# Performance work log

Hardware: AMD Instinct MI355X
Metric: run time of the kernel (lower is better)

Reference implementation:

```python
import jax, jax.numpy as jnp
import numpy as np

N_UNITS = 1024
H = 16
D_K = N_UNITS // H
B = 4
T = 2048


def setup_inputs() -> dict:
    key = jax.random.key(0)
    ks = jax.random.split(key, 9)
    scale = 1.0 / np.sqrt(N_UNITS)
    return {
        "x": jax.random.normal(ks[0], (B * T, N_UNITS), dtype=jnp.float32),
        "Wq": jax.random.normal(ks[1], (N_UNITS, N_UNITS), dtype=jnp.float32) * scale,
        "bq": jax.random.normal(ks[2], (N_UNITS,), dtype=jnp.float32) * 0.01,
        "Wk": jax.random.normal(ks[3], (N_UNITS, N_UNITS), dtype=jnp.float32) * scale,
        "bk": jax.random.normal(ks[4], (N_UNITS,), dtype=jnp.float32) * 0.01,
        "Wv": jax.random.normal(ks[5], (N_UNITS, N_UNITS), dtype=jnp.float32) * scale,
        "bv": jax.random.normal(ks[6], (N_UNITS,), dtype=jnp.float32) * 0.01,
        "Wo": jax.random.normal(ks[7], (N_UNITS, N_UNITS), dtype=jnp.float32) * scale,
        "bo": jax.random.normal(ks[8], (N_UNITS,), dtype=jnp.float32) * 0.01,
        "batch_size": B,
    }


def reference(x, Wq, bq, Wk, bk, Wv, bv, Wo, bo, batch_size):
    # x: (batch*seq, n_units). Project then split into heads.
    q = (x @ Wq.T + bq).reshape(batch_size, -1, H, D_K)  # (b, t, h, d)
    k = (x @ Wk.T + bk).reshape(batch_size, -1, H, D_K)
    v = (x @ Wv.T + bv).reshape(batch_size, -1, H, D_K)
    scores = jnp.einsum("bqhd,bkhd->bhqk", q, k) / np.sqrt(D_K)
    att = jax.nn.softmax(scores, axis=-1)  # dropout=0.0 -> identity
    ctx = jnp.einsum("bhqk,bkhd->bqhd", att, v)
    ctx = ctx.reshape(-1, H * D_K)  # (batch*seq, n_units)
    return ctx @ Wo.T + bo
```

## Files before the change

### kernel.cpp

```cpp
#include <hip/hip_runtime.h>

typedef __bf16 bf16_t;
typedef __attribute__((ext_vector_type(8))) __bf16 bf16x8;
typedef __attribute__((ext_vector_type(4))) __bf16 bf16x4;
typedef __attribute__((ext_vector_type(4))) float f32x4;

#define M_TOT 8192
#define NU    1024
#define TSEQ  2048
#define NHEAD 16
#define DHEAD 64
#define BPAD  72
#define QSCALE 0.18033688011f

__device__ __forceinline__ void gload_lds16(const void* g, void* lds) {
    __builtin_amdgcn_global_load_lds(
        (const __attribute__((address_space(1))) void*)g,
        (__attribute__((address_space(3))) void*)lds,
        16, 0, 0);
}

__device__ __forceinline__ unsigned pk2(float a, float b) {
    const bf16_t x = (bf16_t)a, y = (bf16_t)b;
    return (unsigned)__builtin_bit_cast(unsigned short, x)
         | ((unsigned)__builtin_bit_cast(unsigned short, y) << 16);
}

__device__ __forceinline__ int fidx(int r, int k) {
    return ((((r >> 4) & 3) * 2 + (k >> 5)) << 9)
         + (((((k >> 3) & 3) << 4) + (r & 15)) << 3) + (k & 7);
}
__device__ __forceinline__ size_t fragK(int bh, int t, int d) {
    return (size_t)bh * (TSEQ * DHEAD) + (size_t)(t >> 6) * 4096 + fidx(t & 63, d);
}
__device__ __forceinline__ size_t fragV(int bh, int t, int d) {
    return (size_t)bh * (TSEQ * DHEAD) + (size_t)(t >> 6) * 4096 + fidx(d, t & 63);
}

__global__ __launch_bounds__(256)
void cvt_x(const float* __restrict__ x, bf16_t* __restrict__ xb)
{
    const int i = (blockIdx.x * 256 + threadIdx.x) * 8;
    const float4 a = *(const float4*)(x + i);
    const float4 b = *(const float4*)(x + i + 4);
    bf16x8 v;
    v[0] = (bf16_t)a.x; v[1] = (bf16_t)a.y; v[2] = (bf16_t)a.z; v[3] = (bf16_t)a.w;
    v[4] = (bf16_t)b.x; v[5] = (bf16_t)b.y; v[6] = (bf16_t)b.z; v[7] = (bf16_t)b.w;
    *(bf16x8*)(xb + i) = v;
}

__global__ __launch_bounds__(256)
void cvt_frag2(const float* __restrict__ x,
               const float* __restrict__ Wq, const float* __restrict__ Wk,
               const float* __restrict__ Wv, const float* __restrict__ Wo,
               bf16_t* __restrict__ Xf, bf16_t* __restrict__ Wf4)
{
    const int bid = blockIdx.x;
    const float* src;
    bf16_t* dst;
    int trow, tcol;
    if (bid < 2048) {
        src = x;
        dst = Xf + (size_t)bid * 4096;
        trow = bid >> 4; tcol = bid & 15;
    } else {
        const int t    = bid - 2048;
        const int wsel = t >> 8;
        const int tt   = t & 255;
        src = (wsel == 0) ? Wq : (wsel == 1 ? Wk : (wsel == 2 ? Wv : Wo));
        dst = Wf4 + (size_t)wsel * NU * NU + (size_t)tt * 4096;
        trow = tt >> 4; tcol = tt & 15;
    }
    const size_t row0 = (size_t)trow * 64;
    const int    col0 = tcol * 64;

    const int tid = threadIdx.x;
#pragma unroll
    for (int h = 0; h < 2; ++h) {
        const int chunk = h * 256 + tid;
        const int r  = chunk >> 3;
        const int k8 = chunk & 7;
        const float* s = src + (row0 + r) * NU + col0 + k8 * 8;
        const float4 a = *(const float4*)(s);
        const float4 b = *(const float4*)(s + 4);
        bf16x8 v;
        v[0] = (bf16_t)a.x; v[1] = (bf16_t)a.y; v[2] = (bf16_t)a.z; v[3] = (bf16_t)a.w;
        v[4] = (bf16_t)b.x; v[5] = (bf16_t)b.y; v[6] = (bf16_t)b.z; v[7] = (bf16_t)b.w;
        const int idx = ((((r >> 4) & 3) * 2 + (k8 >> 2)) << 9)
                      + (((k8 & 3) * 16 + (r & 15)) << 3);
        *(bf16x8*)(dst + idx) = v;
    }
}

__global__ __launch_bounds__(256)
void gemm_qkv_f(const bf16_t* __restrict__ xf,
                const bf16_t* __restrict__ Wqf, const bf16_t* __restrict__ Wkf, const bf16_t* __restrict__ Wvf,
                const float* __restrict__ B0, const float* __restrict__ B1, const float* __restrict__ B2,
                bf16_t* __restrict__ O0, bf16_t* __restrict__ O1, bf16_t* __restrict__ O2)
{
    const int z = blockIdx.z;
    const bf16_t* Wf  = (z == 0) ? Wqf : (z == 1 ? Wkf : Wvf);
    const float* bias = (z == 0) ? B0 : (z == 1 ? B1 : B2);
    bf16_t* out       = (z == 0) ? O0 : (z == 1 ? O1 : O2);
    const float scale = (z == 0) ? QSCALE : 1.0f;

    __shared__ __attribute__((aligned(16))) bf16_t S[2][16384];

    const int tid = threadIdx.x;
    const int l   = tid & 63;
    const int w   = tid >> 6;
    const int wm  = w >> 1, wn = w & 1;
    const int l15 = l & 15, lq = l >> 4;

    const int lid = blockIdx.y * 8 + blockIdx.x;
    const int bm  = (lid & 7) * 8 + (lid >> 6);
    const int bn  = (lid >> 3) & 7;

    const bf16_t* gA[4];
    const bf16_t* gB[4];
#pragma unroll
    for (int i = 0; i < 4; ++i) {
        const int cc = w * 4 + i;
        gA[i] = xf + ((size_t)(bm * 2 + (cc >> 3)) * 16) * 4096 + (cc & 7) * 512 + l * 8;
        gB[i] = Wf + ((size_t)(bn * 2 + (cc >> 3)) * 16) * 4096 + (cc & 7) * 512 + l * 8;
    }

#define STAGE_T(b, ktn)                                                          \
    do {                                                                         \
        _Pragma("unroll")                                                        \
        for (int i_ = 0; i_ < 4; ++i_) {                                         \
            const int cc_ = w * 4 + i_;                                          \
            gload_lds16(gA[i_] + (size_t)(ktn) * 4096, &S[b][cc_ * 512]);        \
            gload_lds16(gB[i_] + (size_t)(ktn) * 4096, &S[b][8192 + cc_ * 512]); \
        }                                                                        \
    } while (0)

    f32x4 acc[4][4] = {};

    STAGE_T(0, 0);
    for (int kt = 0; kt < 16; ++kt) {
        const int cur = kt & 1;
        if (kt < 15) {
            STAGE_T(cur ^ 1, kt + 1);
            asm volatile("s_waitcnt vmcnt(8)\n\ts_barrier" ::: "memory");
        } else {
            asm volatile("s_waitcnt vmcnt(0)\n\ts_barrier" ::: "memory");
        }
        const bf16_t* Asb = &S[cur][0];
        const bf16_t* Bsb = &S[cur][8192];
#pragma unroll
        for (int ks = 0; ks < 2; ++ks) {
            bf16x8 af[4], bfr[4];
#pragma unroll
            for (int mt = 0; mt < 4; ++mt)
                af[mt] = *(const bf16x8*)&Asb[wm * 4096 + (mt * 2 + ks) * 512 + l * 8];
#pragma unroll
            for (int nt = 0; nt < 4; ++nt)
                bfr[nt] = *(const bf16x8*)&Bsb[wn * 4096 + (nt * 2 + ks) * 512 + l * 8];
#pragma unroll
            for (int mt = 0; mt < 4; ++mt)
#pragma unroll
                for (int nt = 0; nt < 4; ++nt)
                    acc[mt][nt] = __builtin_amdgcn_mfma_f32_16x16x32_bf16(af[mt], bfr[nt], acc[mt][nt], 0, 0, 0);
        }
    }
#undef STAGE_T

    bf16_t* Cs = &S[0][w * 4096];
#pragma unroll
    for (int nt = 0; nt < 4; ++nt) {
        const int gn = bn * 128 + wn * 64 + nt * 16 + l15;
        const float bv = bias[gn];
        const int kp = nt * 16 + l15;
#pragma unroll
        for (int mt = 0; mt < 4; ++mt) {
#pragma unroll
            for (int r = 0; r < 4; ++r) {
                const int rp = mt * 16 + lq * 4 + r;
                const float v = (acc[mt][nt][r] + bv) * scale;
                int idx;
                if (z == 0)      idx = rp * 64 + kp;
                else if (z == 1) idx = fidx(rp, kp);
                else             idx = fidx(kp, rp);
                Cs[idx] = (bf16_t)v;
            }
        }
    }
    const int bm2 = bm * 2 + wm;
    const int b   = bm2 >> 5;
    const int hh  = bn * 2 + wn;
    const int bh  = b * NHEAD + hh;
    size_t obase;
    if (z == 0) obase = ((size_t)bh * TSEQ + (size_t)(bm2 & 31) * 64) * DHEAD;
    else        obase = ((size_t)bh * 32 + (bm2 & 31)) * 4096;
#pragma unroll
    for (int c = 0; c < 8; ++c) {
        const bf16x8 cv = *(const bf16x8*)&Cs[c * 512 + l * 8];
        *(bf16x8*)(out + obase + c * 512 + l * 8) = cv;
    }
}

__global__ __launch_bounds__(256)
void gemm_out_f(const bf16_t* __restrict__ cf, const bf16_t* __restrict__ Wof,
                const float* __restrict__ bo, float* __restrict__ out)
{
    __shared__ __attribute__((aligned(16))) bf16_t S[2][16384];

    const int tid = threadIdx.x;
    const int l   = tid & 63;
    const int w   = tid >> 6;
    const int wm  = w >> 1, wn = w & 1;
    const int l15 = l & 15, lq = l >> 4;

    const int lid = blockIdx.y * 8 + blockIdx.x;
    const int bm  = (lid & 7) * 8 + (lid >> 6);
    const int bn  = (lid >> 3) & 7;
    const int b   = bm >> 4;

    const bf16_t* gB[4];
    size_t aoff[4];
#pragma unroll
    for (int i = 0; i < 4; ++i) {
        const int cc = w * 4 + i;
        aoff[i] = (((size_t)b * 16) * 32 + (bm & 15) * 2 + (cc >> 3)) * 4096 + (cc & 7) * 512 + l * 8;
        gB[i] = Wof + ((size_t)(bn * 2 + (cc >> 3)) * 16) * 4096 + (cc & 7) * 512 + l * 8;
    }

#define STAGE_O(bf, ktn)                                                                  \
    do {                                                                                  \
        _Pragma("unroll")                                                                 \
        for (int i_ = 0; i_ < 4; ++i_) {                                                  \
            const int cc_ = w * 4 + i_;                                                   \
            gload_lds16(cf + aoff[i_] + (size_t)(ktn) * (32 * 4096), &S[bf][cc_ * 512]);  \
            gload_lds16(gB[i_] + (size_t)(ktn) * 4096, &S[bf][8192 + cc_ * 512]);         \
        }                                                                                 \
    } while (0)

    f32x4 acc[4][4] = {};

    STAGE_O(0, 0);
    for (int kt = 0; kt < 16; ++kt) {
        const int cur = kt & 1;
        if (kt < 15) {
            STAGE_O(cur ^ 1, kt + 1);
            asm volatile("s_waitcnt vmcnt(8)\n\ts_barrier" ::: "memory");
        } else {
            asm volatile("s_waitcnt vmcnt(0)\n\ts_barrier" ::: "memory");
        }
        const bf16_t* Asb = &S[cur][0];
        const bf16_t* Bsb = &S[cur][8192];
#pragma unroll
        for (int ks = 0; ks < 2; ++ks) {
            bf16x8 af[4], bfr[4];
#pragma unroll
            for (int mt = 0; mt < 4; ++mt)
                af[mt] = *(const bf16x8*)&Asb[wm * 4096 + (mt * 2 + ks) * 512 + l * 8];
#pragma unroll
            for (int nt = 0; nt < 4; ++nt)
                bfr[nt] = *(const bf16x8*)&Bsb[wn * 4096 + (nt * 2 + ks) * 512 + l * 8];
#pragma unroll
            for (int mt = 0; mt < 4; ++mt)
#pragma unroll
                for (int nt = 0; nt < 4; ++nt)
                    acc[mt][nt] = __builtin_amdgcn_mfma_f32_16x16x32_bf16(af[mt], bfr[nt], acc[mt][nt], 0, 0, 0);
        }
    }
#undef STAGE_O

#pragma unroll
    for (int nt = 0; nt < 4; ++nt) {
        const int gn = bn * 128 + wn * 64 + nt * 16 + l15;
        const float bv = bo[gn];
#pragma unroll
        for (int mt = 0; mt < 4; ++mt) {
            const int rb = bm * 128 + wm * 64 + mt * 16 + lq * 4;
#pragma unroll
            for (int r = 0; r < 4; ++r)
                out[(size_t)(rb + r) * NU + gn] = acc[mt][nt][r] + bv;
        }
    }
}

__global__ __launch_bounds__(256)
void gemm_qkv(const bf16_t* __restrict__ A,
              const float* __restrict__ W0, const float* __restrict__ W1, const float* __restrict__ W2,
              const float* __restrict__ B0, const float* __restrict__ B1, const float* __restrict__ B2,
              bf16_t* __restrict__ O0, bf16_t* __restrict__ O1, bf16_t* __restrict__ O2)
{
    const int z = blockIdx.z;
    const float* W    = (z == 0) ? W0 : (z == 1 ? W1 : W2);
    const float* bias = (z == 0) ? B0 : (z == 1 ? B1 : B2);
    bf16_t* out       = (z == 0) ? O0 : (z == 1 ? O1 : O2);
    const float scale = (z == 0) ? QSCALE : 1.0f;

    __shared__ __attribute__((aligned(16))) bf16_t As[128 * 64];
    __shared__ __attribute__((aligned(16))) bf16_t Bs[128 * BPAD];

    const int tid = threadIdx.x;
    const int l = tid & 63, w = tid >> 6;
    const int wm = w >> 1, wn = w & 1;
    const int l15 = l & 15, lq = l >> 4;
    const int bm = blockIdx.y, bn = blockIdx.x;
    const int srow = l >> 3, scol = (l & 7) * 8;
    const bf16_t* gA = A + (size_t)(bm * 128 + srow) * NU + scol;
    const int sr = tid >> 4, sc = (tid & 15) * 4;
    const float* gW = W + (size_t)(bn * 128 + sr) * NU + sc;

    f32x4 acc[4][4] = {};
    float4 wreg[8];
#pragma unroll
    for (int i = 0; i < 8; ++i) wreg[i] = *(const float4*)(gW + (size_t)(i * 16) * NU);

    for (int k0 = 0; k0 < NU; k0 += 64) {
#pragma unroll
        for (int i = 0; i < 4; ++i) {
            const int r0 = i * 32 + w * 8;
            gload_lds16(gA + (size_t)r0 * NU + k0, &As[r0 * 64]);
        }
#pragma unroll
        for (int i = 0; i < 8; ++i) {
            bf16x4 wb;
            wb[0] = (bf16_t)wreg[i].x; wb[1] = (bf16_t)wreg[i].y;
            wb[2] = (bf16_t)wreg[i].z; wb[3] = (bf16_t)wreg[i].w;
            *(bf16x4*)&Bs[(i * 16 + sr) * BPAD + sc] = wb;
        }
        __syncthreads();
        if (k0 + 64 < NU) {
#pragma unroll
            for (int i = 0; i < 8; ++i)
                wreg[i] = *(const float4*)(gW + (size_t)(i * 16) * NU + k0 + 64);
        }
#pragma unroll
        for (int ks = 0; ks < 2; ++ks) {
            bf16x8 af[4], bfr[4];
#pragma unroll
            for (int mt = 0; mt < 4; ++mt)
                af[mt] = *(const bf16x8*)&As[(wm * 64 + mt * 16 + l15) * 64 + ks * 32 + lq * 8];
#pragma unroll
            for (int nt = 0; nt < 4; ++nt)
                bfr[nt] = *(const bf16x8*)&Bs[(wn * 64 + nt * 16 + l15) * BPAD + ks * 32 + lq * 8];
#pragma unroll
            for (int mt = 0; mt < 4; ++mt)
#pragma unroll
                for (int nt = 0; nt < 4; ++nt)
                    acc[mt][nt] = __builtin_amdgcn_mfma_f32_16x16x32_bf16(af[mt], bfr[nt], acc[mt][nt], 0, 0, 0);
        }
        __syncthreads();
    }

#pragma unroll
    for (int nt = 0; nt < 4; ++nt) {
        const int gn = bn * 128 + wn * 64 + nt * 16 + l15;
        const float bv = bias[gn];
#pragma unroll
        for (int mt = 0; mt < 4; ++mt) {
            const int rb = bm * 128 + wm * 64 + mt * 16 + lq * 4;
#pragma unroll
            for (int r = 0; r < 4; ++r) {
                const int gm = rb + r;
                const float v = (acc[mt][nt][r] + bv) * scale;
                const int b = gm >> 11, t = gm & (TSEQ - 1);
                const int h = gn >> 6,  d = gn & 63;
                const int bh = b * NHEAD + h;
                if (z == 0)      out[((size_t)bh * TSEQ + t) * DHEAD + d] = (bf16_t)v;
                else if (z == 1) out[fragK(bh, t, d)] = (bf16_t)v;
                else             out[fragV(bh, t, d)] = (bf16_t)v;
            }
        }
    }
}

__global__ __launch_bounds__(256)
void gemm_out(const bf16_t* __restrict__ ctx, const float* __restrict__ Wo,
              const float* __restrict__ bo, float* __restrict__ out)
{
    __shared__ __attribute__((aligned(16))) bf16_t As[128 * 64];
    __shared__ __attribute__((aligned(16))) bf16_t Bs[128 * BPAD];

    const int tid = threadIdx.x;
    const int l = tid & 63, w = tid >> 6;
    const int wm = w >> 1, wn = w & 1;
    const int l15 = l & 15, lq = l >> 4;
    const int bm = blockIdx.y, bn = blockIdx.x;
    const int srow = l >> 3, scol = (l & 7) * 8;
    const int b = bm >> 4;
    const bf16_t* gA = ctx + (size_t)b * (NHEAD * TSEQ * DHEAD)
                           + (size_t)((bm & 15) * 128 + srow) * DHEAD + scol;
    const int sr = tid >> 4, sc = (tid & 15) * 4;
    const float* gW = Wo + (size_t)(bn * 128 + sr) * NU + sc;

    f32x4 acc[4][4] = {};
    float4 wreg[8];
#pragma unroll
    for (int i = 0; i < 8; ++i) wreg[i] = *(const float4*)(gW + (size_t)(i * 16) * NU);

    for (int k0 = 0; k0 < NU; k0 += 64) {
#pragma unroll
        for (int i = 0; i < 4; ++i) {
            const int r0 = i * 32 + w * 8;
            gload_lds16(gA + (size_t)r0 * DHEAD + ((size_t)k0 << 11), &As[r0 * 64]);
        }
#pragma unroll
        for (int i = 0; i < 8; ++i) {
            bf16x4 wb;
            wb[0] = (bf16_t)wreg[i].x; wb[1] = (bf16_t)wreg[i].y;
            wb[2] = (bf16_t)wreg[i].z; wb[3] = (bf16_t)wreg[i].w;
            *(bf16x4*)&Bs[(i * 16 + sr) * BPAD + sc] = wb;
        }
        __syncthreads();
        if (k0 + 64 < NU) {
#pragma unroll
            for (int i = 0; i < 8; ++i)
                wreg[i] = *(const float4*)(gW + (size_t)(i * 16) * NU + k0 + 64);
        }
#pragma unroll
        for (int ks = 0; ks < 2; ++ks) {
            bf16x8 af[4], bfr[4];
#pragma unroll
            for (int mt = 0; mt < 4; ++mt)
                af[mt] = *(const bf16x8*)&As[(wm * 64 + mt * 16 + l15) * 64 + ks * 32 + lq * 8];
#pragma unroll
            for (int nt = 0; nt < 4; ++nt)
                bfr[nt] = *(const bf16x8*)&Bs[(wn * 64 + nt * 16 + l15) * BPAD + ks * 32 + lq * 8];
#pragma unroll
            for (int mt = 0; mt < 4; ++mt)
#pragma unroll
                for (int nt = 0; nt < 4; ++nt)
                    acc[mt][nt] = __builtin_amdgcn_mfma_f32_16x16x32_bf16(af[mt], bfr[nt], acc[mt][nt], 0, 0, 0);
        }
        __syncthreads();
    }

#pragma unroll
    for (int nt = 0; nt < 4; ++nt) {
        const int gn = bn * 128 + wn * 64 + nt * 16 + l15;
        const float bv = bo[gn];
#pragma unroll
        for (int mt = 0; mt < 4; ++mt) {
            const int rb = bm * 128 + wm * 64 + mt * 16 + lq * 4;
#pragma unroll
            for (int r = 0; r < 4; ++r)
                out[(size_t)(rb + r) * NU + gn] = acc[mt][nt][r] + bv;
        }
    }
}

template <bool FRAGOUT>
__global__ __launch_bounds__(256, 3)
void attn_fwd(const bf16_t* __restrict__ Q, const bf16_t* __restrict__ Kf,
              const bf16_t* __restrict__ Vf, bf16_t* __restrict__ Cw)
{
    __shared__ __attribute__((aligned(16))) bf16_t Ps[4][4 * 512];

    const int tid = threadIdx.x;
    const int l   = tid & 63;
    const int w   = tid >> 6;
    const int l15 = l & 15, lq = l >> 4;

    const int id = blockIdx.x;
    const int bh = (id & 7) * 8 + ((id >> 3) & 7);
    const int qt = id >> 6;
    const int q0 = qt * 128 + w * 32;

    const bf16_t* Qb = Q  + (size_t)bh * TSEQ * DHEAD;
    const bf16_t* Kb = Kf + (size_t)bh * TSEQ * DHEAD + l * 8;
    const bf16_t* Vb = Vf + (size_t)bh * TSEQ * DHEAD + l * 8;

    bf16x8 qf[2][2];
#pragma unroll
    for (int mt = 0; mt < 2; ++mt)
#pragma unroll
        for (int ks = 0; ks < 2; ++ks)
            qf[mt][ks] = *(const bf16x8*)(Qb + (size_t)(q0 + mt * 16 + l15) * DHEAD + ks * 32 + lq * 8);

    bf16x8 ones;
#pragma unroll
    for (int j = 0; j < 8; ++j) ones[j] = (bf16_t)1.0f;

    f32x4 cacc[2][4] = {};
    f32x4 lacc[2] = {};

    int* PsI = (int*)&Ps[w][0];

    for (int kt = 0; kt < TSEQ / 64; ++kt) {
        const bf16_t* kb = Kb + kt * 4096;
        const bf16_t* vb = Vb + kt * 4096;

        bf16x8 kf[8];
#pragma unroll
        for (int c = 0; c < 8; ++c) kf[c] = *(const bf16x8*)(kb + c * 512);

        f32x4 st[4][2] = {};
#pragma unroll
        for (int ks = 0; ks < 2; ++ks)
#pragma unroll
            for (int nt = 0; nt < 4; ++nt)
#pragma unroll
                for (int mt = 0; mt < 2; ++mt)
                    st[nt][mt] = __builtin_amdgcn_mfma_f32_16x16x32_bf16(kf[nt * 2 + ks], qf[mt][ks], st[nt][mt], 0, 0, 0);

#pragma unroll
        for (int nt = 0; nt < 4; ++nt)
#pragma unroll
            for (int mt = 0; mt < 2; ++mt) {
                const float p0 = __builtin_amdgcn_exp2f(st[nt][mt][0]);
                const float p1 = __builtin_amdgcn_exp2f(st[nt][mt][1]);
                const float p2 = __builtin_amdgcn_exp2f(st[nt][mt][2]);
                const float p3 = __builtin_amdgcn_exp2f(st[nt][mt][3]);
                const int base = (mt * 2 + (nt >> 1)) * 256
                               + ((nt & 1) * 2 + (lq >> 1)) * 64 + l15 * 4;
                PsI[base + ((lq * 2 + 0) & 3)] = (int)pk2(p0, p1);
                PsI[base + ((lq * 2 + 1) & 3)] = (int)pk2(p2, p3);
            }

        bf16x8 vf[8];
#pragma unroll
        for (int c = 0; c < 8; ++c) vf[c] = *(const bf16x8*)(vb + c * 512);

#pragma unroll
        for (int kv = 0; kv < 2; ++kv) {
            bf16x8 pf[2];
#pragma unroll
            for (int mt = 0; mt < 2; ++mt)
                pf[mt] = *(const bf16x8*)&Ps[w][(mt * 2 + kv) * 512 + l * 8];
#pragma unroll
            for (int mt = 0; mt < 2; ++mt) {
                lacc[mt] = __builtin_amdgcn_mfma_f32_16x16x32_bf16(ones, pf[mt], lacc[mt], 0, 0, 0);
#pragma unroll
                for (int dt = 0; dt < 4; ++dt)
                    cacc[mt][dt] = __builtin_amdgcn_mfma_f32_16x16x32_bf16(vf[dt * 2 + kv], pf[mt], cacc[mt][dt], 0, 0, 0);
            }
        }
    }

#pragma unroll
    for (int mt = 0; mt < 2; ++mt) {
        const float inv = 1.0f / lacc[mt][0];
        const int q = q0 + mt * 16 + l15;
#pragma unroll
        for (int dt = 0; dt < 4; ++dt) {
            bf16x4 cv;
#pragma unroll
            for (int r = 0; r < 4; ++r) cv[r] = (bf16_t)(cacc[mt][dt][r] * inv);
            if (FRAGOUT) {
                const int qr = q & 63;
                const size_t base = ((size_t)bh * 32 + (q >> 6)) * 4096;
                const int d0 = dt * 16 + lq * 4;
                const int addr = ((((qr >> 4) & 3) * 2 + (d0 >> 5)) << 9)
                               + (((((d0 >> 3) & 3) << 4) + (qr & 15)) << 3) + (d0 & 7);
                *(bf16x4*)&Cw[base + addr] = cv;
            } else {
                *(bf16x4*)&Cw[((size_t)bh * TSEQ + q) * DHEAD + dt * 16 + lq * 4] = cv;
            }
        }
    }
}

__global__ void diag_fill(float* out, int n, float val)
{
    int i = blockIdx.x * blockDim.x + threadIdx.x;
    if (i < n) out[i] = val;
}

extern "C" void kernel_launch(void* const* d_in, const int* in_sizes, int n_in,
                              void* d_out, int out_size, void* d_ws, size_t ws_size,
                              hipStream_t stream)
{
    const float* x  = (const float*)d_in[0];
    const float* Wq = (const float*)d_in[1];
    const float* bq = (const float*)d_in[2];
    const float* Wk = (const float*)d_in[3];
    const float* bk = (const float*)d_in[4];
    const float* Wv = (const float*)d_in[5];
    const float* bv = (const float*)d_in[6];
    const float* Wo = (const float*)d_in[7];
    const float* bo = (const float*)d_in[8];

    const size_t SLOT = (size_t)M_TOT * NU;
    const size_t WSZ  = (size_t)NU * NU;
    const size_t need_fast = (2 * SLOT + 4 * WSZ) * sizeof(bf16_t);
    const size_t need_min  = 2 * SLOT * sizeof(bf16_t);

    bf16_t* Qw = (bf16_t*)d_out;
    bf16_t* Kw = Qw + SLOT;

    if (ws_size >= need_fast) {
        bf16_t* Xf  = (bf16_t*)d_ws;
        bf16_t* Vt  = Xf + SLOT;
        bf16_t* Wf4 = Vt + SLOT;
        bf16_t* Cf  = Xf;

        cvt_frag2<<<dim3(2048 + 4 * 256), 256, 0, stream>>>(x, Wq, Wk, Wv, Wo, Xf, Wf4);
        gemm_qkv_f<<<dim3(NU / 128, M_TOT / 128, 3), 256, 0, stream>>>(
            Xf, Wf4, Wf4 + WSZ, Wf4 + 2 * WSZ, bq, bk, bv, Qw, Kw, Vt);
        attn_fwd<true><<<dim3(1024), 256, 0, stream>>>(Qw, Kw, Vt, Cf);
        gemm_out_f<<<dim3(NU / 128, M_TOT / 128), 256, 0, stream>>>(Cf, Wf4 + 3 * WSZ, bo, (float*)d_out);
    } else if (ws_size >= need_min) {
        bf16_t* Xb = (bf16_t*)d_ws;
        bf16_t* Vt = Xb + SLOT;
        bf16_t* Cw = Xb;
        cvt_x<<<dim3(M_TOT * NU / (256 * 8)), 256, 0, stream>>>(x, Xb);
        gemm_qkv<<<dim3(NU / 128, M_TOT / 128, 3), 256, 0, stream>>>(
            Xb, Wq, Wk, Wv, bq, bk, bv, Qw, Kw, Vt);
        attn_fwd<false><<<dim3(1024), 256, 0, stream>>>(Qw, Kw, Vt, Cw);
        gemm_out<<<dim3(NU / 128, M_TOT / 128), 256, 0, stream>>>(Cw, Wo, bo, (float*)d_out);
    } else {
        diag_fill<<<(out_size + 255) / 256, 256, 0, stream>>>((float*)d_out, out_size, 9.0f);
    }
}
```

Baseline: 266.4 us.

## Enlarge QKV GEMM tile to 256x256 with 512-thread blocks and XCD-aware mapping

The fused QKV projection GEMM moves from 128x128 tiles on 256-thread blocks to 256x256 tiles on 512-thread blocks. Each wave now computes 128x64 outputs, and the three projections are packed into a 1D grid of 384 blocks with an XCD-aware block-to-tile mapping. The larger tile doubles operand reuse per LDS load and cuts global traffic per FLOP. It also raises LDS use to 128 KB per block, so at most one block fits on a CU, and 384 blocks spread unevenly over the CUs. A trailing barrier is added to the k-loops of both GEMMs so the next prefetch cannot overwrite a buffer that slower waves are still reading.

```diff
diff --git a/kernel.cpp b/kernel.cpp
--- a/kernel.cpp
+++ b/kernel.cpp
@@ -92,111 +92,109 @@
     }
 }
 
-__global__ __launch_bounds__(256)
+__global__ __launch_bounds__(512, 2)
 void gemm_qkv_f(const bf16_t* __restrict__ xf,
                 const bf16_t* __restrict__ Wqf, const bf16_t* __restrict__ Wkf, const bf16_t* __restrict__ Wvf,
                 const float* __restrict__ B0, const float* __restrict__ B1, const float* __restrict__ B2,
                 bf16_t* __restrict__ O0, bf16_t* __restrict__ O1, bf16_t* __restrict__ O2)
 {
-    const int z = blockIdx.z;
+    __shared__ __attribute__((aligned(16))) bf16_t S[2][32768];
+
+    const int tid = threadIdx.x;
+    const int l   = tid & 63;
+    const int w   = tid >> 6;
+    const int wm  = w >> 2, wn = w & 3;
+    const int l15 = l & 15, lq = l >> 4;
+
+    const int lid = blockIdx.x;
+    const int xcd = lid & 7;
+    const int j   = lid >> 3;
+    const int z   = j >> 4;
+    const int jj  = j & 15;
+    const int bm  = xcd * 4 + (jj & 3);
+    const int bn  = jj >> 2;
+
     const bf16_t* Wf  = (z == 0) ? Wqf : (z == 1 ? Wkf : Wvf);
     const float* bias = (z == 0) ? B0 : (z == 1 ? B1 : B2);
     bf16_t* out       = (z == 0) ? O0 : (z == 1 ? O1 : O2);
     const float scale = (z == 0) ? QSCALE : 1.0f;
 
-    __shared__ __attribute__((aligned(16))) bf16_t S[2][16384];
-
-    const int tid = threadIdx.x;
-    const int l   = tid & 63;
-    const int w   = tid >> 6;
-    const int wm  = w >> 1, wn = w & 1;
-    const int l15 = l & 15, lq = l >> 4;
-
-    const int lid = blockIdx.y * 8 + blockIdx.x;
-    const int bm  = (lid & 7) * 8 + (lid >> 6);
-    const int bn  = (lid >> 3) & 7;
-
-    const bf16_t* gA[4];
-    const bf16_t* gB[4];
-#pragma unroll
-    for (int i = 0; i < 4; ++i) {
-        const int cc = w * 4 + i;
-        gA[i] = xf + ((size_t)(bm * 2 + (cc >> 3)) * 16) * 4096 + (cc & 7) * 512 + l * 8;
-        gB[i] = Wf + ((size_t)(bn * 2 + (cc >> 3)) * 16) * 4096 + (cc & 7) * 512 + l * 8;
-    }
-
-#define STAGE_T(b, ktn)                                                          \
-    do {                                                                         \
-        _Pragma("unroll")                                                        \
-        for (int i_ = 0; i_ < 4; ++i_) {                                         \
-            const int cc_ = w * 4 + i_;                                          \
-            gload_lds16(gA[i_] + (size_t)(ktn) * 4096, &S[b][cc_ * 512]);        \
-            gload_lds16(gB[i_] + (size_t)(ktn) * 4096, &S[b][8192 + cc_ * 512]); \
-        }                                                                        \
+    const bf16_t* gsrc = (w < 4)
+        ? xf + ((size_t)(bm * 4 + w) * 16) * 4096 + l * 8
+        : Wf + ((size_t)(bn * 4 + (w - 4)) * 16) * 4096 + l * 8;
+
+#define STAGE_Q(bf, ktn)                                                      \
+    do {                                                                      \
+        _Pragma("unroll")                                                     \
+        for (int i_ = 0; i_ < 8; ++i_)                                        \
+            gload_lds16(gsrc + (size_t)(ktn) * 4096 + i_ * 512,               \
+                        &S[bf][(w * 8 + i_) * 512]);                          \
     } while (0)
 
-    f32x4 acc[4][4] = {};
-
-    STAGE_T(0, 0);
+    f32x4 acc[8][4] = {};
+
+    STAGE_Q(0, 0);
     for (int kt = 0; kt < 16; ++kt) {
         const int cur = kt & 1;
         if (kt < 15) {
-            STAGE_T(cur ^ 1, kt + 1);
+            STAGE_Q(cur ^ 1, kt + 1);
             asm volatile("s_waitcnt vmcnt(8)\n\ts_barrier" ::: "memory");
         } else {
             asm volatile("s_waitcnt vmcnt(0)\n\ts_barrier" ::: "memory");
         }
         const bf16_t* Asb = &S[cur][0];
-        const bf16_t* Bsb = &S[cur][8192];
+        const bf16_t* Bsb = &S[cur][16384];
 #pragma unroll
         for (int ks = 0; ks < 2; ++ks) {
-            bf16x8 af[4], bfr[4];
-#pragma unroll
-            for (int mt = 0; mt < 4; ++mt)
-                af[mt] = *(const bf16x8*)&Asb[wm * 4096 + (mt * 2 + ks) * 512 + l * 8];
+            bf16x8 af[8], bfr[4];
+#pragma unroll
+            for (int mt = 0; mt < 8; ++mt)
+                af[mt] = *(const bf16x8*)&Asb[(wm * 2 + (mt >> 2)) * 4096 + ((mt & 3) * 2 + ks) * 512 + l * 8];
 #pragma unroll
             for (int nt = 0; nt < 4; ++nt)
                 bfr[nt] = *(const bf16x8*)&Bsb[wn * 4096 + (nt * 2 + ks) * 512 + l * 8];
 #pragma unroll
-            for (int mt = 0; mt < 4; ++mt)
+            for (int mt = 0; mt < 8; ++mt)
 #pragma unroll
                 for (int nt = 0; nt < 4; ++nt)
                     acc[mt][nt] = __builtin_amdgcn_mfma_f32_16x16x32_bf16(af[mt], bfr[nt], acc[mt][nt], 0, 0, 0);
         }
-    }
-#undef STAGE_T
+        asm volatile("s_barrier" ::: "memory");
+    }
+#undef STAGE_Q
 
     bf16_t* Cs = &S[0][w * 4096];
-#pragma unroll
-    for (int nt = 0; nt < 4; ++nt) {
-        const int gn = bn * 128 + wn * 64 + nt * 16 + l15;
-        const float bv = bias[gn];
-        const int kp = nt * 16 + l15;
-#pragma unroll
-        for (int mt = 0; mt < 4; ++mt) {
-#pragma unroll
-            for (int r = 0; r < 4; ++r) {
-                const int rp = mt * 16 + lq * 4 + r;
-                const float v = (acc[mt][nt][r] + bv) * scale;
-                int idx;
-                if (z == 0)      idx = rp * 64 + kp;
-                else if (z == 1) idx = fidx(rp, kp);
-                else             idx = fidx(kp, rp);
-                Cs[idx] = (bf16_t)v;
+    const int head = bn * 4 + wn;
+#pragma unroll
+    for (int p = 0; p < 2; ++p) {
+#pragma unroll
+        for (int nt = 0; nt < 4; ++nt) {
+            const int kp = nt * 16 + l15;
+            const float bv = bias[head * 64 + kp];
+#pragma unroll
+            for (int m4 = 0; m4 < 4; ++m4) {
+#pragma unroll
+                for (int r = 0; r < 4; ++r) {
+                    const int rp = m4 * 16 + lq * 4 + r;
+                    const float v = (acc[p * 4 + m4][nt][r] + bv) * scale;
+                    int idx;
+                    if (z == 0)      idx = rp * 64 + kp;
+                    else if (z == 1) idx = fidx(rp, kp);
+                    else             idx = fidx(kp, rp);
+                    Cs[idx] = (bf16_t)v;
+                }
             }
         }
-    }
-    const int bm2 = bm * 2 + wm;
-    const int b   = bm2 >> 5;
-    const int hh  = bn * 2 + wn;
-    const int bh  = b * NHEAD + hh;
-    size_t obase;
-    if (z == 0) obase = ((size_t)bh * TSEQ + (size_t)(bm2 & 31) * 64) * DHEAD;
-    else        obase = ((size_t)bh * 32 + (bm2 & 31)) * 4096;
-#pragma unroll
-    for (int c = 0; c < 8; ++c) {
-        const bf16x8 cv = *(const bf16x8*)&Cs[c * 512 + l * 8];
-        *(bf16x8*)(out + obase + c * 512 + l * 8) = cv;
+        const int bm2 = bm * 4 + wm * 2 + p;
+        const int bh  = (bm2 >> 5) * NHEAD + head;
+        const size_t obase = (z == 0)
+            ? (size_t)bh * (TSEQ * DHEAD) + (size_t)(bm2 & 31) * 4096
+            : ((size_t)bh * 32 + (bm2 & 31)) * 4096;
+#pragma unroll
+        for (int c = 0; c < 8; ++c) {
+            const bf16x8 cv = *(const bf16x8*)&Cs[c * 512 + l * 8];
+            *(bf16x8*)(out + obase + c * 512 + l * 8) = cv;
+        }
     }
 }
 
@@ -264,6 +262,7 @@
                 for (int nt = 0; nt < 4; ++nt)
                     acc[mt][nt] = __builtin_amdgcn_mfma_f32_16x16x32_bf16(af[mt], bfr[nt], acc[mt][nt], 0, 0, 0);
         }
+        asm volatile("s_barrier" ::: "memory");
     }
 #undef STAGE_O
 
@@ -591,7 +590,7 @@
         bf16_t* Cf  = Xf;
 
         cvt_frag2<<<dim3(2048 + 4 * 256), 256, 0, stream>>>(x, Wq, Wk, Wv, Wo, Xf, Wf4);
-        gemm_qkv_f<<<dim3(NU / 128, M_TOT / 128, 3), 256, 0, stream>>>(
+        gemm_qkv_f<<<dim3(384), 512, 0, stream>>>(
             Xf, Wf4, Wf4 + WSZ, Wf4 + 2 * WSZ, bq, bk, bv, Qw, Kw, Vt);
         attn_fwd<true><<<dim3(1024), 256, 0, stream>>>(Qw, Kw, Vt, Cf);
         gemm_out_f<<<dim3(NU / 128, M_TOT / 128), 256, 0, stream>>>(Cf, Wf4 + 3 * WSZ, bo, (float*)d_out);
```

Measured after the change: 273.6 us. 2.7% more time.
